# Performance work log

Measured on AMD Instinct MI355X. Metric: run time of the kernel, lower is better.

The kernel has to match this reference:

```python
import jax, jax.numpy as jnp
import numpy as np

IN_FEATURES = 1024
OUT_FEATURES = 64
KERNEL_DIMS = 16
N = 512


def setup_inputs() -> dict:
    key = jax.random.key(0)
    kx, kT = jax.random.split(key)
    x = jax.random.normal(kx, (N, IN_FEATURES), dtype=jnp.float32)
    T = jax.random.normal(kT, (IN_FEATURES, OUT_FEATURES, KERNEL_DIMS), dtype=jnp.float32)
    return {"x": x, "T": T}


def reference(x, T):
    n = x.shape[0]
    # Project: [N, in] @ [in, out*kd] -> [N, out, kd]
    matrices = (x @ T.reshape(T.shape[0], -1)).reshape(n, OUT_FEATURES, KERNEL_DIMS)
    # Pairwise L1 distance over kernel dims: [N, N, out]
    norm = jnp.abs(matrices[None, :, :, :] - matrices[:, None, :, :]).sum(axis=3)
    expnorm = jnp.exp(-norm)
    # Exclude self-similarity (diagonal) and sum over the batch axis
    mask = 1.0 - jnp.eye(n, dtype=x.dtype)
    o_b = (expnorm * mask[:, :, None]).sum(axis=1)  # [N, out]
    return jnp.concatenate([x, o_b], axis=1)
```

## Files before the change

kernel.cpp:

```cpp
#include <hip/hip_runtime.h>
#include <hip/hip_bf16.h>
#include <hip/hip_fp16.h>

#define NB     512
#define INF    1024
#define OUTF   64
#define PROJ   1024
#define OROW   (INF + OUTF)

typedef short short8 __attribute__((ext_vector_type(8)));
typedef float floatx4 __attribute__((ext_vector_type(4)));

#define SA 36
#define SB 68

__device__ __forceinline__ unsigned pack_bf16(float x, float y) {
    __hip_bfloat162 h = __float22bfloat162_rn(make_float2(x, y));
    union { __hip_bfloat162 h; unsigned u; } v; v.h = h; return v.u;
}

__device__ __forceinline__ __half2 as_h2(unsigned u) {
    union { unsigned u; __half2 h; } v; v.u = u; return v.h;
}

__global__ __launch_bounds__(256, 2) void gemm_fused(const float* __restrict__ A,
                                                     const float* __restrict__ B,
                                                     float* __restrict__ out,
                                                     __half* __restrict__ M16) {
    __shared__ unsigned As[16 * SA];
    __shared__ unsigned Bs[32 * SB];

    const int t    = threadIdx.x;
    const int lane = t & 63, w = t >> 6;
    const int bnx = blockIdx.x, bmy = blockIdx.y;
    const int bm = bmy * 16, bn = bnx * 64;

    {
        const int r = t >> 4, c4 = (t & 15) * 4;
        *(float4*)&out[(size_t)(bm + r) * OROW + bn + c4] =
            *(const float4*)&A[(size_t)(bm + r) * INF + bn + c4];
    }
    if (t < 16) {
        const int row = bmy * 16 + bnx;
        *(float4*)&out[(size_t)row * OROW + INF + t * 4] =
            make_float4(-1.f, -1.f, -1.f, -1.f);
    }

    const int am  = t >> 4;
    const int ak  = (t & 15) * 4;
    const int bkp = t >> 4;
    const int bn0 = (t & 15) * 4;

    const int q = lane >> 4, c = lane & 15;
    const unsigned* apo = &As[c * SA + q * 4];
    const unsigned* bpo = &Bs[(q * 4) * SB + w * 16 + c];

    floatx4 acc = {0.f, 0.f, 0.f, 0.f};

    const size_t aoff  = (size_t)(bm + am) * INF + ak;
    const float* Bbase = B + bn + bn0;

    float4 av  = *(const float4*)&A[aoff];
    float4 b0a = *(const float4*)&Bbase[(size_t)(2 * bkp)      * PROJ];
    float4 b0b = *(const float4*)&Bbase[(size_t)(2 * bkp + 1)  * PROJ];
    float4 b1a = *(const float4*)&Bbase[(size_t)(2 * bkp + 32) * PROJ];
    float4 b1b = *(const float4*)&Bbase[(size_t)(2 * bkp + 33) * PROJ];

    for (int k0 = 0; k0 < INF; k0 += 64) {
        __syncthreads();
        *(uint2*)&As[am * SA + (ak >> 1)] =
            make_uint2(pack_bf16(av.x, av.y), pack_bf16(av.z, av.w));
        *(uint4*)&Bs[bkp * SB + bn0] =
            make_uint4(pack_bf16(b0a.x, b0b.x), pack_bf16(b0a.y, b0b.y),
                       pack_bf16(b0a.z, b0b.z), pack_bf16(b0a.w, b0b.w));
        *(uint4*)&Bs[(bkp + 16) * SB + bn0] =
            make_uint4(pack_bf16(b1a.x, b1b.x), pack_bf16(b1a.y, b1b.y),
                       pack_bf16(b1a.z, b1b.z), pack_bf16(b1a.w, b1b.w));
        __syncthreads();

        const int kn = k0 + 64;
        if (kn < INF) {
            av  = *(const float4*)&A[aoff + kn];
            b0a = *(const float4*)&Bbase[(size_t)(kn + 2 * bkp)      * PROJ];
            b0b = *(const float4*)&Bbase[(size_t)(kn + 2 * bkp + 1)  * PROJ];
            b1a = *(const float4*)&Bbase[(size_t)(kn + 2 * bkp + 32) * PROJ];
            b1b = *(const float4*)&Bbase[(size_t)(kn + 2 * bkp + 33) * PROJ];
        }

        union { uint4 u; short8 s; } alo, ahi;
        alo.u = *(const uint4*)(apo);
        ahi.u = *(const uint4*)(apo + 16);
        union { unsigned u[4]; short8 s; } blo, bhi;
#pragma unroll
        for (int j = 0; j < 4; ++j) {
            blo.u[j] = bpo[j * SB];
            bhi.u[j] = bpo[(j + 16) * SB];
        }
        acc = __builtin_amdgcn_mfma_f32_16x16x32_bf16(alo.s, blo.s, acc, 0, 0, 0);
        acc = __builtin_amdgcn_mfma_f32_16x16x32_bf16(ahi.s, bhi.s, acc, 0, 0, 0);
    }

#pragma unroll
    for (int r = 0; r < 4; ++r) {
        M16[(size_t)(bm + q * 4 + r) * PROJ + bn + w * 16 + c] = __float2half(acc[r]);
    }
}

__device__ __forceinline__ float l1norm16(const uint4 a0, const uint4 a1,
                                          const uint4 b0, const uint4 b1) {
    __half2 s0 = __hadd2(__habs2(__hsub2(as_h2(a0.x), as_h2(b0.x))),
                         __habs2(__hsub2(as_h2(a0.y), as_h2(b0.y))));
    __half2 s1 = __hadd2(__habs2(__hsub2(as_h2(a0.z), as_h2(b0.z))),
                         __habs2(__hsub2(as_h2(a0.w), as_h2(b0.w))));
    __half2 s2 = __hadd2(__habs2(__hsub2(as_h2(a1.x), as_h2(b1.x))),
                         __habs2(__hsub2(as_h2(a1.y), as_h2(b1.y))));
    __half2 s3 = __hadd2(__habs2(__hsub2(as_h2(a1.z), as_h2(b1.z))),
                         __habs2(__hsub2(as_h2(a1.w), as_h2(b1.w))));
    const __half2 s = __hadd2(__hadd2(s0, s1), __hadd2(s2, s3));
    return __low2float(s) + __high2float(s);
}

__global__ __launch_bounds__(128) void pairwise_h2(const __half* __restrict__ M16,
                                                   float* __restrict__ out) {
    __shared__ __half Mj[64 * 64];

    const int t  = threadIdx.x;
    const int o  = t & 3;
    const int il = t >> 2;
    const int og = blockIdx.x;
    const int ig = blockIdx.y;
    const int j0 = blockIdx.z * 64;
    const int ia = ig * 64 + il;
    const int ib = ia + 32;

    const uint4* mpa = (const uint4*)&M16[(size_t)ia * PROJ + og * 64 + o * 16];
    const uint4* mpb = (const uint4*)&M16[(size_t)ib * PROJ + og * 64 + o * 16];
    const uint4 a0 = mpa[0], a1 = mpa[1];
    const uint4 a2 = mpb[0], a3 = mpb[1];

#pragma unroll
    for (int cc = 0; cc < 4; ++cc) {
        const int idx = (cc * 128 + t) * 8;
        const int jl  = idx >> 6;
        const int col = idx & 63;
        *(uint4*)&Mj[jl * 64 + col] =
            *(const uint4*)&M16[(size_t)(j0 + jl) * PROJ + og * 64 + col];
    }
    __syncthreads();

    float sa0 = 0.f, sa1 = 0.f, sb0 = 0.f, sb1 = 0.f;
#pragma unroll 4
    for (int jl = 0; jl < 64; ++jl) {
        const uint4 b0 = *(const uint4*)&Mj[jl * 64 + o * 16];
        const uint4 b1 = *(const uint4*)&Mj[jl * 64 + o * 16 + 8];
        const float na = l1norm16(a0, a1, b0, b1);
        const float nb = l1norm16(a2, a3, b0, b1);
        if (jl & 1) { sa1 += __expf(-na); sb1 += __expf(-nb); }
        else        { sa0 += __expf(-na); sb0 += __expf(-nb); }
    }

    __hip_atomic_fetch_add(&out[(size_t)ia * OROW + INF + og * 4 + o],
                           sa0 + sa1, __ATOMIC_RELAXED, __HIP_MEMORY_SCOPE_AGENT);
    __hip_atomic_fetch_add(&out[(size_t)ib * OROW + INF + og * 4 + o],
                           sb0 + sb1, __ATOMIC_RELAXED, __HIP_MEMORY_SCOPE_AGENT);
}

extern "C" void kernel_launch(void* const* d_in, const int* in_sizes, int n_in,
                              void* d_out, int out_size, void* d_ws, size_t ws_size,
                              hipStream_t stream) {
    const float* x = (const float*)d_in[0];
    const float* T = (const float*)d_in[1];
    float* out  = (float*)d_out;
    __half* M16 = (__half*)d_ws;

    gemm_fused<<<dim3(PROJ / 64, NB / 16), 256, 0, stream>>>(x, T, out, M16);
    pairwise_h2<<<dim3(OUTF / 4, NB / 64, NB / 64), 128, 0, stream>>>(M16, out);
}
```

Measured before the change: 88.94 us.

## Exploit pairwise symmetry and enlarge GEMM tile to 32x64 with 512 threads

The pairwise kernel now visits only upper-triangular 64x64 tile pairs. Each off-diagonal tile adds its exp-distance sums to both the i rows and the j rows, using shuffle reductions and a shared buffer, which roughly halves the L1/exp work. The GEMM moves to 32-row tiles with 512 threads and a transposed B staging layout, so the fragments come from single vector LDS reads. The cost is extra shuffles, shared-memory writes and atomics, plus a small triangular index loop per block.

```diff
diff --git a/kernel.cpp b/kernel.cpp
--- a/kernel.cpp
+++ b/kernel.cpp
@@ -12,7 +12,7 @@
 typedef float floatx4 __attribute__((ext_vector_type(4)));
 
 #define SA 36
-#define SB 68
+#define SB 36
 
 __device__ __forceinline__ unsigned pack_bf16(float x, float y) {
     __hip_bfloat162 h = __float22bfloat162_rn(make_float2(x, y));
@@ -23,86 +23,84 @@
     union { unsigned u; __half2 h; } v; v.u = u; return v.h;
 }
 
-__global__ __launch_bounds__(256, 2) void gemm_fused(const float* __restrict__ A,
+__global__ __launch_bounds__(512, 1) void gemm_fused(const float* __restrict__ A,
                                                      const float* __restrict__ B,
                                                      float* __restrict__ out,
                                                      __half* __restrict__ M16) {
-    __shared__ unsigned As[16 * SA];
-    __shared__ unsigned Bs[32 * SB];
+    __shared__ unsigned As[32 * SA];
+    __shared__ unsigned Bs[64 * SB];
 
     const int t    = threadIdx.x;
     const int lane = t & 63, w = t >> 6;
     const int bnx = blockIdx.x, bmy = blockIdx.y;
-    const int bm = bmy * 16, bn = bnx * 64;
+    const int bm = bmy * 32, bn = bnx * 64;
 
     {
         const int r = t >> 4, c4 = (t & 15) * 4;
         *(float4*)&out[(size_t)(bm + r) * OROW + bn + c4] =
             *(const float4*)&A[(size_t)(bm + r) * INF + bn + c4];
     }
-    if (t < 16) {
-        const int row = bmy * 16 + bnx;
-        *(float4*)&out[(size_t)row * OROW + INF + t * 4] =
+    if (t < 32) {
+        const int row = (bmy * 16 + bnx) * 2 + (t >> 4);
+        *(float4*)&out[(size_t)row * OROW + INF + (t & 15) * 4] =
             make_float4(-1.f, -1.f, -1.f, -1.f);
     }
 
-    const int am  = t >> 4;
-    const int ak  = (t & 15) * 4;
-    const int bkp = t >> 4;
-    const int bn0 = (t & 15) * 4;
+    const int am = t >> 3, ak = (t & 7) * 8;
+    const int g  = w,      n0 = t & 63;
 
     const int q = lane >> 4, c = lane & 15;
-    const unsigned* apo = &As[c * SA + q * 4];
-    const unsigned* bpo = &Bs[(q * 4) * SB + w * 16 + c];
+    const int mt = w >> 2, nq = w & 3;
+    const unsigned* ap = &As[(mt * 16 + c) * SA + q * 4];
+    const unsigned* bp = &Bs[(nq * 16 + c) * SB + q * 4];
 
     floatx4 acc = {0.f, 0.f, 0.f, 0.f};
 
-    const size_t aoff  = (size_t)(bm + am) * INF + ak;
-    const float* Bbase = B + bn + bn0;
-
-    float4 av  = *(const float4*)&A[aoff];
-    float4 b0a = *(const float4*)&Bbase[(size_t)(2 * bkp)      * PROJ];
-    float4 b0b = *(const float4*)&Bbase[(size_t)(2 * bkp + 1)  * PROJ];
-    float4 b1a = *(const float4*)&Bbase[(size_t)(2 * bkp + 32) * PROJ];
-    float4 b1b = *(const float4*)&Bbase[(size_t)(2 * bkp + 33) * PROJ];
+    const float* Acol = A + (size_t)(bm + am) * INF + ak;
+    const float* Bcol = B + bn + n0;
+
+    float4 av0, av1;
+    if (t < 256) { av0 = *(const float4*)(Acol); av1 = *(const float4*)(Acol + 4); }
+    float bv[8];
+#pragma unroll
+    for (int e = 0; e < 8; ++e) bv[e] = Bcol[(size_t)(g * 8 + e) * PROJ];
 
     for (int k0 = 0; k0 < INF; k0 += 64) {
         __syncthreads();
-        *(uint2*)&As[am * SA + (ak >> 1)] =
-            make_uint2(pack_bf16(av.x, av.y), pack_bf16(av.z, av.w));
-        *(uint4*)&Bs[bkp * SB + bn0] =
-            make_uint4(pack_bf16(b0a.x, b0b.x), pack_bf16(b0a.y, b0b.y),
-                       pack_bf16(b0a.z, b0b.z), pack_bf16(b0a.w, b0b.w));
-        *(uint4*)&Bs[(bkp + 16) * SB + bn0] =
-            make_uint4(pack_bf16(b1a.x, b1b.x), pack_bf16(b1a.y, b1b.y),
-                       pack_bf16(b1a.z, b1b.z), pack_bf16(b1a.w, b1b.w));
+        if (t < 256) {
+            *(uint4*)&As[am * SA + (ak >> 1)] =
+                make_uint4(pack_bf16(av0.x, av0.y), pack_bf16(av0.z, av0.w),
+                           pack_bf16(av1.x, av1.y), pack_bf16(av1.z, av1.w));
+        }
+        *(uint4*)&Bs[n0 * SB + g * 4] =
+            make_uint4(pack_bf16(bv[0], bv[1]), pack_bf16(bv[2], bv[3]),
+                       pack_bf16(bv[4], bv[5]), pack_bf16(bv[6], bv[7]));
         __syncthreads();
 
         const int kn = k0 + 64;
         if (kn < INF) {
-            av  = *(const float4*)&A[aoff + kn];
-            b0a = *(const float4*)&Bbase[(size_t)(kn + 2 * bkp)      * PROJ];
-            b0b = *(const float4*)&Bbase[(size_t)(kn + 2 * bkp + 1)  * PROJ];
-            b1a = *(const float4*)&Bbase[(size_t)(kn + 2 * bkp + 32) * PROJ];
-            b1b = *(const float4*)&Bbase[(size_t)(kn + 2 * bkp + 33) * PROJ];
+            if (t < 256) {
+                av0 = *(const float4*)(Acol + kn);
+                av1 = *(const float4*)(Acol + kn + 4);
+            }
+#pragma unroll
+            for (int e = 0; e < 8; ++e)
+                bv[e] = Bcol[(size_t)(kn + g * 8 + e) * PROJ];
         }
 
-        union { uint4 u; short8 s; } alo, ahi;
-        alo.u = *(const uint4*)(apo);
-        ahi.u = *(const uint4*)(apo + 16);
-        union { unsigned u[4]; short8 s; } blo, bhi;
-#pragma unroll
-        for (int j = 0; j < 4; ++j) {
-            blo.u[j] = bpo[j * SB];
-            bhi.u[j] = bpo[(j + 16) * SB];
-        }
+        union { uint4 u; short8 s; } alo, ahi, blo, bhi;
+        alo.u = *(const uint4*)(ap);
+        ahi.u = *(const uint4*)(ap + 16);
+        blo.u = *(const uint4*)(bp);
+        bhi.u = *(const uint4*)(bp + 16);
         acc = __builtin_amdgcn_mfma_f32_16x16x32_bf16(alo.s, blo.s, acc, 0, 0, 0);
         acc = __builtin_amdgcn_mfma_f32_16x16x32_bf16(ahi.s, bhi.s, acc, 0, 0, 0);
     }
 
 #pragma unroll
     for (int r = 0; r < 4; ++r) {
-        M16[(size_t)(bm + q * 4 + r) * PROJ + bn + w * 16 + c] = __float2half(acc[r]);
+        M16[(size_t)(bm + mt * 16 + q * 4 + r) * PROJ + bn + nq * 16 + c] =
+            __float2half(acc[r]);
     }
 }
 
@@ -120,17 +118,25 @@
     return __low2float(s) + __high2float(s);
 }
 
-__global__ __launch_bounds__(128) void pairwise_h2(const __half* __restrict__ M16,
-                                                   float* __restrict__ out) {
-    __shared__ __half Mj[64 * 64];
-
-    const int t  = threadIdx.x;
-    const int o  = t & 3;
-    const int il = t >> 2;
-    const int og = blockIdx.x;
-    const int ig = blockIdx.y;
-    const int j0 = blockIdx.z * 64;
-    const int ia = ig * 64 + il;
+__global__ __launch_bounds__(128) void pairwise_sym(const __half* __restrict__ M16,
+                                                    float* __restrict__ out) {
+    __shared__ __half Mj[32 * 64];
+    __shared__ float jsum[32 * 8];
+
+    const int t    = threadIdx.x;
+    const int o    = t & 3;
+    const int il   = t >> 2;
+    const int w    = t >> 6;
+    const int og   = blockIdx.y;
+    const int jh   = blockIdx.z;
+
+    int ti = 0, rem = blockIdx.x;
+    while (rem >= 8 - ti) { rem -= 8 - ti; ++ti; }
+    const int tj = ti + rem;
+    const bool diag = (ti == tj);
+
+    const int j0 = tj * 64 + jh * 32;
+    const int ia = ti * 64 + il;
     const int ib = ia + 32;
 
     const uint4* mpa = (const uint4*)&M16[(size_t)ia * PROJ + og * 64 + o * 16];
@@ -139,7 +145,7 @@
     const uint4 a2 = mpb[0], a3 = mpb[1];
 
 #pragma unroll
-    for (int cc = 0; cc < 4; ++cc) {
+    for (int cc = 0; cc < 2; ++cc) {
         const int idx = (cc * 128 + t) * 8;
         const int jl  = idx >> 6;
         const int col = idx & 63;
@@ -150,19 +156,36 @@
 
     float sa0 = 0.f, sa1 = 0.f, sb0 = 0.f, sb1 = 0.f;
 #pragma unroll 4
-    for (int jl = 0; jl < 64; ++jl) {
+    for (int jl = 0; jl < 32; ++jl) {
         const uint4 b0 = *(const uint4*)&Mj[jl * 64 + o * 16];
         const uint4 b1 = *(const uint4*)&Mj[jl * 64 + o * 16 + 8];
         const float na = l1norm16(a0, a1, b0, b1);
         const float nb = l1norm16(a2, a3, b0, b1);
-        if (jl & 1) { sa1 += __expf(-na); sb1 += __expf(-nb); }
-        else        { sa0 += __expf(-na); sb0 += __expf(-nb); }
+        const float ea = __expf(-na);
+        const float eb = __expf(-nb);
+        if (jl & 1) { sa1 += ea; sb1 += eb; }
+        else        { sa0 += ea; sb0 += eb; }
+        if (!diag) {
+            float jc = ea + eb;
+            jc += __shfl_xor(jc, 4);
+            jc += __shfl_xor(jc, 8);
+            jc += __shfl_xor(jc, 16);
+            jc += __shfl_xor(jc, 32);
+            jsum[jl * 8 + o * 2 + w] = jc;
+        }
     }
 
     __hip_atomic_fetch_add(&out[(size_t)ia * OROW + INF + og * 4 + o],
                            sa0 + sa1, __ATOMIC_RELAXED, __HIP_MEMORY_SCOPE_AGENT);
     __hip_atomic_fetch_add(&out[(size_t)ib * OROW + INF + og * 4 + o],
                            sb0 + sb1, __ATOMIC_RELAXED, __HIP_MEMORY_SCOPE_AGENT);
+
+    if (!diag) {
+        __syncthreads();
+        const float v = jsum[2 * t] + jsum[2 * t + 1];
+        __hip_atomic_fetch_add(&out[(size_t)(j0 + (t >> 2)) * OROW + INF + og * 4 + (t & 3)],
+                               v, __ATOMIC_RELAXED, __HIP_MEMORY_SCOPE_AGENT);
+    }
 }
 
 extern "C" void kernel_launch(void* const* d_in, const int* in_sizes, int n_in,
@@ -173,6 +196,6 @@
     float* out  = (float*)d_out;
     __half* M16 = (__half*)d_ws;
 
-    gemm_fused<<<dim3(PROJ / 64, NB / 16), 256, 0, stream>>>(x, T, out, M16);
-    pairwise_h2<<<dim3(OUTF / 4, NB / 64, NB / 64), 128, 0, stream>>>(M16, out);
-}
+    gemm_fused<<<dim3(PROJ / 64, NB / 32), 512, 0, stream>>>(x, T, out, M16);
+    pairwise_sym<<<dim3(36, 16, 2), 128, 0, stream>>>(M16, out);
+}
```

New measurement: 86.50 us. 1.03x faster.
